# Optimization experiments

Hardware: AMD Instinct MI355X
Metric: run time of the kernel (lower is better)

## Reference

```python
import jax, jax.numpy as jnp
import numpy as np
from jax import lax

D, H_HEADS, DEPTH, E, HID, P, NCLS = 768, 12, 12, 4, 3072, 16, 1000

def _ln(x, w, b, eps=1e-5):
    m = x.mean(-1, keepdims=True)
    v = ((x - m) ** 2).mean(-1, keepdims=True)
    return (x - m) * lax.rsqrt(v + eps) * w + b

def setup_inputs() -> dict:
    key = jax.random.key(0)
    ks = jax.random.split(key, 16)
    s = 0.02
    inp = {
        'x': jax.random.normal(ks[0], (32, 3, 224, 224), jnp.float32),
        'conv_w': jax.random.normal(ks[1], (D, 3, P, P), jnp.float32) * s,
        'conv_b': jnp.zeros((D,), jnp.float32),
        'cls_token': jnp.zeros((1, 1, D), jnp.float32),
        'pos_embed': jax.random.normal(ks[2], (1, 197, D), jnp.float32) * s,
        'ln1_w': jnp.ones((DEPTH, D), jnp.float32),
        'ln1_b': jnp.zeros((DEPTH, D), jnp.float32),
        'qkv_w': jax.random.normal(ks[3], (DEPTH, 3 * D, D), jnp.float32) * s,
        'qkv_b': jnp.zeros((DEPTH, 3 * D), jnp.float32),
        'out_w': jax.random.normal(ks[4], (DEPTH, D, D), jnp.float32) * s,
        'out_b': jnp.zeros((DEPTH, D), jnp.float32),
        'ln2_w': jnp.ones((DEPTH, D), jnp.float32),
        'ln2_b': jnp.zeros((DEPTH, D), jnp.float32),
        'gate_w': jax.random.normal(ks[5], (DEPTH, E, D), jnp.float32) * s,
        'gate_b': jnp.zeros((DEPTH, E), jnp.float32),
        'e1_w': jax.random.normal(ks[6], (DEPTH, E, HID, D), jnp.float32) * s,
        'e1_b': jnp.zeros((DEPTH, E, HID), jnp.float32),
        'e2_w': jax.random.normal(ks[7], (DEPTH, E, D, HID), jnp.float32) * s,
        'e2_b': jnp.zeros((DEPTH, E, D), jnp.float32),
        'fnorm_w': jnp.ones((D,), jnp.float32),
        'fnorm_b': jnp.zeros((D,), jnp.float32),
        'head_w': jax.random.normal(ks[8], (NCLS, D), jnp.float32) * s,
        'head_b': jnp.zeros((NCLS,), jnp.float32),
    }
    return inp

def reference(x, conv_w, conv_b, cls_token, pos_embed, ln1_w, ln1_b, qkv_w, qkv_b,
              out_w, out_b, ln2_w, ln2_b, gate_w, gate_b, e1_w, e1_b, e2_w, e2_b,
              fnorm_w, fnorm_b, head_w, head_b):
    B = x.shape[0]
    # patch embedding: conv stride=patch, then flatten -> [B, N, D]
    x = lax.conv_general_dilated(x, conv_w, (P, P), 'VALID',
                                 dimension_numbers=('NCHW', 'OIHW', 'NCHW'))
    x = x + conv_b[None, :, None, None]
    x = x.reshape(B, D, -1).transpose(0, 2, 1)
    x = jnp.concatenate([jnp.broadcast_to(cls_token, (B, 1, D)), x], axis=1)
    x = x + pos_embed
    N = x.shape[1]
    hd = D // H_HEADS
    for i in range(DEPTH):
        # --- attention ---
        h = x
        y = _ln(x, ln1_w[i], ln1_b[i])
        qkv = y @ qkv_w[i].T + qkv_b[i]                      # [B,N,3D]
        q, k, v = jnp.split(qkv, 3, axis=-1)
        q = q.reshape(B, N, H_HEADS, hd).transpose(0, 2, 1, 3) / jnp.sqrt(hd).astype(x.dtype)
        k = k.reshape(B, N, H_HEADS, hd).transpose(0, 2, 1, 3)
        v = v.reshape(B, N, H_HEADS, hd).transpose(0, 2, 1, 3)
        attn = jax.nn.softmax(jnp.einsum('bhqd,bhkd->bhqk', q, k), axis=-1)
        ctx = jnp.einsum('bhqk,bhkd->bhqd', attn, v).transpose(0, 2, 1, 3).reshape(B, N, D)
        x = h + (ctx @ out_w[i].T + out_b[i])
        # --- MoE MLP (dense: all experts computed then masked, top_k=1) ---
        h = x
        y = _ln(x, ln2_w[i], ln2_b[i])
        gate = y @ gate_w[i].T + gate_b[i]                   # [B,N,E]
        topk_scores, topk_idx = lax.top_k(gate, 1)           # [B,N,1]
        score = jax.nn.softmax(topk_scores, axis=-1)[..., 0]  # [B,N] (==1 for k=1)
        h1 = jax.nn.gelu(jnp.einsum('bnd,ehd->benh', y, e1_w[i])
                         + e1_b[i][None, :, None, :], approximate=False)  # [B,E,N,HID]
        oe = jnp.einsum('benh,edh->bend', h1, e2_w[i]) + e2_b[i][None, :, None, :]
        mask = jax.nn.one_hot(topk_idx[..., 0], E, dtype=y.dtype)  # [B,N,E]
        moe = jnp.einsum('bne,bend->bnd', mask * score[..., None], oe)
        x = h + moe
    x = _ln(x, fnorm_w, fnorm_b)
    cls = x[:, 0]
    return cls @ head_w.T + head_b
```

## Files before the change

### kernel.cpp

```cpp
#include <hip/hip_runtime.h>
#include <hip/hip_bf16.h>
#include <math.h>

#define D_MODEL 768
#define SEQ     197
#define BATCH   32
#define NTOK    (BATCH*SEQ)
#define NHEAD   12
#define HDIM    64
#define NEXP    4
#define HID_N   3072
#define DEPTH_N 12

typedef __attribute__((ext_vector_type(4))) float f32x4;
typedef __attribute__((ext_vector_type(8))) short bf16x8;
typedef __attribute__((ext_vector_type(4))) unsigned short u16x4;
typedef unsigned short u16;

static __device__ __forceinline__ u16 f2bf(float f){
  unsigned int u = __builtin_bit_cast(unsigned int, f);
  u += 0x7FFFu + ((u >> 16) & 1u);
  return (u16)(u >> 16);
}
static __device__ __forceinline__ void split_bf(float x, u16& h, u16& l){
  h = f2bf(x);
  float hf = __builtin_bit_cast(float, (unsigned)h << 16);
  l = f2bf(x - hf);
}

static __device__ __forceinline__ float wred_sum(float v){
  #pragma unroll
  for (int off = 32; off; off >>= 1) v += __shfl_down(v, off);
  return v;
}

static __device__ __forceinline__ void gld16(const u16* g, u16* l){
  __builtin_amdgcn_global_load_lds(
      (const __attribute__((address_space(1))) unsigned int*)g,
      (__attribute__((address_space(3))) unsigned int*)l, 16, 0, 0);
}

__global__ __launch_bounds__(256) void split_many(const float* __restrict__ src,
                                                  u16* __restrict__ hi,
                                                  u16* __restrict__ lo, long n4){
  for (long i = blockIdx.x*256L + threadIdx.x; i < n4; i += (long)gridDim.x*256){
    f32x4 v = *reinterpret_cast<const f32x4*>(src + i*4);
    u16x4 h, l;
    #pragma unroll
    for (int j = 0; j < 4; j++){ u16 hh, ll; split_bf(v[j], hh, ll); h[j]=hh; l[j]=ll; }
    *reinterpret_cast<u16x4*>(hi + i*4) = h;
    *reinterpret_cast<u16x4*>(lo + i*4) = l;
  }
}

template<int MODE, int NG>
__global__ __launch_bounds__(256, 2) void gemm_split(
    const u16* __restrict__ Ahp, const u16* __restrict__ Alp,
    const u16* __restrict__ Whp, const u16* __restrict__ Wlp,
    const float* __restrict__ bias, const float* __restrict__ resid,
    float* __restrict__ C, const float* __restrict__ pos,
    u16* __restrict__ Chi, u16* __restrict__ Clo,
    const int* __restrict__ toks, const int* __restrict__ cnts,
    const int* __restrict__ offs, const int* __restrict__ tiles,
    int MTg, int NBg, int M, int N, int K)
{
  const int tid = threadIdx.x;
  const int NB = N >> 7;
  const int xcd = blockIdx.x & 7;
  const int idx = blockIdx.x >> 3;
  const int mg = xcd / NG, ng = xcd - mg*NG;
  const int mt = mg*MTg + idx / NBg;
  const int nb = ng*NBg + idx % NBg;
  if (nb >= NB) return;

  int cnt = M, base = 0, m0;
  if (MODE == 2 || MODE == 3){
    if (mt >= tiles[0]) return;
    const int e = tiles[1 + 2*mt];
    m0 = tiles[2 + 2*mt];
    cnt  = cnts[e];
    base = offs[e];
    Whp  += (size_t)e * N * K;
    Wlp  += (size_t)e * N * K;
    bias += (size_t)e * N;
  } else {
    m0 = mt * 128;
    if (m0 >= M) return;
  }
  const int n0 = nb * 128;

  __shared__ __align__(16) u16 lds[2][4][4096];

  const int lane = tid & 63, wid = tid >> 6;
  const int i0 = wid*128 + lane;
  const int r0 = i0 >> 2, r1 = r0 + 16;
  const int x0 = (i0 & 3) ^ ((r0 >> 1) & 3);
  const int x1 = (i0 & 3) ^ ((r1 >> 1) & 3);
  const int d0 = wid*1024, d1 = wid*1024 + 512;

  size_t aA0 = 0, aA1 = 0, pb0 = 0, pb1 = 0;
  {
    const int gm0 = m0 + r0, gm1 = m0 + r1;
    if (MODE == 0 || MODE == 1){
      aA0 = (size_t)(gm0 < M ? gm0 : 0) * K + x0*8;
      aA1 = (size_t)(gm1 < M ? gm1 : 0) * K + x1*8;
    }
    if (MODE == 2){
      aA0 = (size_t)(gm0 < cnt ? toks[base+gm0] : 0) * K + x0*8;
      aA1 = (size_t)(gm1 < cnt ? toks[base+gm1] : 0) * K + x1*8;
    }
    if (MODE == 3){
      aA0 = (size_t)(gm0 < cnt ? base+gm0 : 0) * K + x0*8;
      aA1 = (size_t)(gm1 < cnt ? base+gm1 : 0) * K + x1*8;
    }
    if (MODE == 4){
      int b_ = gm0 / 196, pp = gm0 - b_*196;
      pb0 = (size_t)b_*150528 + (size_t)(pp/14)*3584 + (size_t)(pp%14)*16;
      b_ = gm1 / 196; pp = gm1 - b_*196;
      pb1 = (size_t)b_*150528 + (size_t)(pp/14)*3584 + (size_t)(pp%14)*16;
    }
  }
  const size_t aW0 = (size_t)(n0 + r0) * K + x0*8;
  const size_t aW1 = (size_t)(n0 + r1) * K + x1*8;

  auto STAGE = [&](int buf, int t){
    const int k0 = t * 32;
    if (MODE == 4){
      const int kq0 = k0 + x0*8, kq1 = k0 + x1*8;
      size_t a0 = pb0 + (size_t)(kq0>>8)*50176 + (size_t)((kq0>>4)&15)*224 + (size_t)(kq0&15);
      size_t a1 = pb1 + (size_t)(kq1>>8)*50176 + (size_t)((kq1>>4)&15)*224 + (size_t)(kq1&15);
      gld16(Ahp + a0, &lds[buf][0][d0]); gld16(Ahp + a1, &lds[buf][0][d1]);
      gld16(Alp + a0, &lds[buf][1][d0]); gld16(Alp + a1, &lds[buf][1][d1]);
    } else {
      gld16(Ahp + aA0 + k0, &lds[buf][0][d0]); gld16(Ahp + aA1 + k0, &lds[buf][0][d1]);
      gld16(Alp + aA0 + k0, &lds[buf][1][d0]); gld16(Alp + aA1 + k0, &lds[buf][1][d1]);
    }
    gld16(Whp + aW0 + k0, &lds[buf][2][d0]); gld16(Whp + aW1 + k0, &lds[buf][2][d1]);
    gld16(Wlp + aW0 + k0, &lds[buf][3][d0]); gld16(Wlp + aW1 + k0, &lds[buf][3][d1]);
  };

  const int wr = wid >> 1, wc = wid & 1;
  const int lr = lane & 15, lq = lane >> 4;
  int cA[4], cW[4];
  #pragma unroll
  for (int mi = 0; mi < 4; mi++){
    int ra = wr*64 + mi*16 + lr;
    cA[mi] = (4*ra + (lq ^ ((ra>>1)&3))) * 8;
  }
  #pragma unroll
  for (int nj = 0; nj < 4; nj++){
    int rw = wc*64 + nj*16 + lr;
    cW[nj] = (4*rw + (lq ^ ((rw>>1)&3))) * 8;
  }

  const int NT = K >> 5;
  f32x4 acc[4][4] = {};

  STAGE(0, 0);
  for (int t = 0; t < NT; t++){
    const int buf = t & 1;
    if (t + 1 < NT){
      STAGE(buf ^ 1, t + 1);
      asm volatile("s_waitcnt vmcnt(8)" ::: "memory");
    } else {
      asm volatile("s_waitcnt vmcnt(0)" ::: "memory");
    }
    __builtin_amdgcn_s_barrier();
    asm volatile("" ::: "memory");
    const u16* L = &lds[buf][0][0];
    bf16x8 afh[4], afl[4], bfh[4], bfl[4];
    #pragma unroll
    for (int mi = 0; mi < 4; mi++){
      afh[mi] = *reinterpret_cast<const bf16x8*>(L + cA[mi]);
      afl[mi] = *reinterpret_cast<const bf16x8*>(L + 4096 + cA[mi]);
    }
    #pragma unroll
    for (int nj = 0; nj < 4; nj++){
      bfh[nj] = *reinterpret_cast<const bf16x8*>(L + 2*4096 + cW[nj]);
      bfl[nj] = *reinterpret_cast<const bf16x8*>(L + 3*4096 + cW[nj]);
    }
    #pragma unroll
    for (int mi = 0; mi < 4; mi++)
      #pragma unroll
      for (int nj = 0; nj < 4; nj++){
        acc[mi][nj] = __builtin_amdgcn_mfma_f32_16x16x32_bf16(afh[mi], bfh[nj], acc[mi][nj], 0, 0, 0);
        acc[mi][nj] = __builtin_amdgcn_mfma_f32_16x16x32_bf16(afh[mi], bfl[nj], acc[mi][nj], 0, 0, 0);
        acc[mi][nj] = __builtin_amdgcn_mfma_f32_16x16x32_bf16(afl[mi], bfh[nj], acc[mi][nj], 0, 0, 0);
      }
    asm volatile("" ::: "memory");
    __builtin_amdgcn_s_barrier();
  }

  #pragma unroll
  for (int nj = 0; nj < 4; nj++){
    const int ncol = n0 + wc*64 + nj*16 + lr;
    const float bv = bias[ncol];
    #pragma unroll
    for (int mi = 0; mi < 4; mi++){
      const int mb = m0 + wr*64 + mi*16 + lq*4;
      #pragma unroll
      for (int j = 0; j < 4; j++){
        const int m = mb + j;
        float v = acc[mi][nj][j] + bv;
        if (MODE == 0){
          if (m < M) C[(size_t)m * N + ncol] = v;
        }
        if (MODE == 1){
          if (m < M) C[(size_t)m * N + ncol] = v + resid[(size_t)m * N + ncol];
        }
        if (MODE == 2){
          if (m < cnt){
            v = 0.5f * v * (1.f + erff(v * 0.70710678118f));
            u16 h, l; split_bf(v, h, l);
            Chi[(size_t)(base + m) * N + ncol] = h;
            Clo[(size_t)(base + m) * N + ncol] = l;
          }
        }
        if (MODE == 3){
          if (m < cnt){
            int tok = toks[base + m];
            C[(size_t)tok * N + ncol] += v;
          }
        }
        if (MODE == 4){
          int b_ = m / 196, pp = m - b_ * 196;
          C[((size_t)b_ * 197 + 1 + pp) * D_MODEL + ncol] =
              v + pos[(size_t)(1 + pp) * D_MODEL + ncol];
        }
      }
    }
  }
}

__global__ __launch_bounds__(256) void cls_init(const float* __restrict__ cls_tk,
                                                const float* __restrict__ pos,
                                                float* __restrict__ xt){
  const int b = blockIdx.x, tid = threadIdx.x;
  for (int d = tid; d < D_MODEL; d += 256)
    xt[((size_t)b*SEQ)*D_MODEL + d] = cls_tk[d] + pos[d];
}

__global__ __launch_bounds__(256) void ln_kernel(const float* __restrict__ x, size_t xstride,
                                                 const float* __restrict__ w,
                                                 const float* __restrict__ b,
                                                 float* __restrict__ y, size_t ystride,
                                                 u16* __restrict__ yh, u16* __restrict__ yl){
  const int t = blockIdx.x;
  const int tid = threadIdx.x;
  const float* row = x + (size_t)t*xstride;
  float v0 = row[tid], v1 = row[tid+256], v2 = row[tid+512];
  __shared__ float red[4];
  float s = wred_sum(v0+v1+v2);
  if ((tid & 63) == 0) red[tid>>6] = s;
  __syncthreads();
  const float mean = (red[0]+red[1]+red[2]+red[3]) * (1.f/768.f);
  const float d0 = v0-mean, d1 = v1-mean, d2 = v2-mean;
  __syncthreads();
  float q = wred_sum(d0*d0 + d1*d1 + d2*d2);
  if ((tid & 63) == 0) red[tid>>6] = q;
  __syncthreads();
  const float var = (red[0]+red[1]+red[2]+red[3]) * (1.f/768.f);
  const float inv = rsqrtf(var + 1e-5f);
  float o0 = d0*inv*w[tid]     + b[tid];
  float o1 = d1*inv*w[tid+256] + b[tid+256];
  float o2 = d2*inv*w[tid+512] + b[tid+512];
  float* yr = y + (size_t)t*ystride;
  yr[tid] = o0; yr[tid+256] = o1; yr[tid+512] = o2;
  if (yh){
    u16 h, l;
    size_t rb = (size_t)t*768;
    split_bf(o0, h, l); yh[rb+tid]     = h; yl[rb+tid]     = l;
    split_bf(o1, h, l); yh[rb+tid+256] = h; yl[rb+tid+256] = l;
    split_bf(o2, h, l); yh[rb+tid+512] = h; yl[rb+tid+512] = l;
  }
}

__global__ __launch_bounds__(256, 3) void attn_f32(const float* __restrict__ qkv,
                                                   u16* __restrict__ ctxh,
                                                   u16* __restrict__ ctxl){
  const int qt = blockIdx.x, h = blockIdx.y, b = blockIdx.z;
  const int tid = threadIdx.x;
  const int tx = tid & 15, ty = tid >> 4;
  __shared__ float Qs[64][65];
  __shared__ float KPs[64][65];
  __shared__ float Vs[64][65];
  const size_t rs = 3*D_MODEL;
  const float* base = qkv + (size_t)b*SEQ*rs + (size_t)h*HDIM;

  #pragma unroll
  for (int it = 0; it < 16; it++){
    int idx = tid + it*256;
    int r = idx >> 6, c = idx & 63;
    int gq = qt*64 + r;
    float v = (gq < SEQ) ? base[(size_t)gq*rs + c] : 0.f;
    Qs[r][c] = v * 0.125f;
  }
  float m_run[4], l_run[4], o[4][4];
  #pragma unroll
  for (int i = 0; i < 4; i++){
    m_run[i] = -3.0e38f; l_run[i] = 0.f;
    #pragma unroll
    for (int j = 0; j < 4; j++) o[i][j] = 0.f;
  }
  __syncthreads();

  for (int kt = 0; kt < 4; kt++){
    #pragma unroll
    for (int it = 0; it < 16; it++){
      int idx = tid + it*256;
      int r = idx >> 6, c = idx & 63;
      int gk = kt*64 + r;
      float kv = (gk < SEQ) ? base[(size_t)gk*rs + D_MODEL   + c] : 0.f;
      float vv = (gk < SEQ) ? base[(size_t)gk*rs + 2*D_MODEL + c] : 0.f;
      KPs[r][c] = kv;
      Vs[r][c]  = vv;
    }
    __syncthreads();
    float s[4][4] = {};
    for (int d = 0; d < 64; d++){
      float qv[4], kv2[4];
      #pragma unroll
      for (int i = 0; i < 4; i++) qv[i]  = Qs[ty*4+i][d];
      #pragma unroll
      for (int j = 0; j < 4; j++) kv2[j] = KPs[tx*4+j][d];
      #pragma unroll
      for (int i = 0; i < 4; i++)
        #pragma unroll
        for (int j = 0; j < 4; j++) s[i][j] += qv[i]*kv2[j];
    }
    #pragma unroll
    for (int j = 0; j < 4; j++){
      if (kt*64 + tx*4 + j >= SEQ){
        #pragma unroll
        for (int i = 0; i < 4; i++) s[i][j] = -3.0e38f;
      }
    }
    float scale[4];
    #pragma unroll
    for (int i = 0; i < 4; i++){
      float mt = fmaxf(fmaxf(s[i][0], s[i][1]), fmaxf(s[i][2], s[i][3]));
      #pragma unroll
      for (int msk = 1; msk <= 8; msk <<= 1) mt = fmaxf(mt, __shfl_xor(mt, msk));
      float mnew = fmaxf(m_run[i], mt);
      scale[i] = __expf(m_run[i] - mnew);
      float ls = 0.f;
      #pragma unroll
      for (int j = 0; j < 4; j++){ s[i][j] = __expf(s[i][j] - mnew); ls += s[i][j]; }
      #pragma unroll
      for (int msk = 1; msk <= 8; msk <<= 1) ls += __shfl_xor(ls, msk);
      l_run[i] = l_run[i]*scale[i] + ls;
      m_run[i] = mnew;
    }
    __syncthreads();
    #pragma unroll
    for (int i = 0; i < 4; i++)
      #pragma unroll
      for (int j = 0; j < 4; j++) KPs[ty*4+i][tx*4+j] = s[i][j];
    __syncthreads();
    #pragma unroll
    for (int i = 0; i < 4; i++)
      #pragma unroll
      for (int j = 0; j < 4; j++) o[i][j] *= scale[i];
    for (int k = 0; k < 64; k++){
      float pv[4], vv[4];
      #pragma unroll
      for (int i = 0; i < 4; i++) pv[i] = KPs[ty*4+i][k];
      #pragma unroll
      for (int j = 0; j < 4; j++) vv[j] = Vs[k][tx*4+j];
      #pragma unroll
      for (int i = 0; i < 4; i++)
        #pragma unroll
        for (int j = 0; j < 4; j++) o[i][j] += pv[i]*vv[j];
    }
    __syncthreads();
  }
  #pragma unroll
  for (int i = 0; i < 4; i++){
    int q = qt*64 + ty*4 + i;
    if (q < SEQ){
      float inv = 1.f / l_run[i];
      #pragma unroll
      for (int j = 0; j < 4; j++){
        u16 hh, ll;
        split_bf(o[i][j]*inv, hh, ll);
        size_t idx = ((size_t)(b*SEQ + q))*D_MODEL + h*HDIM + tx*4 + j;
        ctxh[idx] = hh; ctxl[idx] = ll;
      }
    }
  }
}

__global__ __launch_bounds__(256) void gate_kernel(const float* __restrict__ y,
                                                   const float* __restrict__ gw,
                                                   const float* __restrict__ gb,
                                                   int* __restrict__ eidx,
                                                   int* __restrict__ counts){
  const int t = blockIdx.x;
  const int tid = threadIdx.x;
  const int e = tid >> 6, lane = tid & 63;
  const float* row = y + (size_t)t*D_MODEL;
  const float* wrow = gw + (size_t)e*D_MODEL;
  float acc = 0.f;
  for (int k = lane; k < D_MODEL; k += 64) acc += row[k]*wrow[k];
  acc = wred_sum(acc);
  __shared__ float sc[NEXP];
  if (lane == 0) sc[e] = acc + gb[e];
  __syncthreads();
  if (tid == 0){
    int best = 0; float bv = sc[0];
    #pragma unroll
    for (int k = 1; k < NEXP; k++) if (sc[k] > bv){ bv = sc[k]; best = k; }
    eidx[t] = best;
    atomicAdd(&counts[best], 1);
  }
}

__global__ void zero_counts(int* c){ if (threadIdx.x < 3*NEXP) c[threadIdx.x] = 0; }

__global__ void offsets_kernel(const int* counts, int* offs, int* cursor, int* tiles){
  if (threadIdx.x == 0){
    int o = 0, n = 0;
    for (int e = 0; e < NEXP; e++){
      offs[e] = o; cursor[e] = o;
      for (int m0 = 0; m0 < counts[e]; m0 += 128){
        tiles[1+2*n] = e; tiles[2+2*n] = m0; n++;
      }
      o += counts[e];
    }
    tiles[0] = n;
  }
}

__global__ __launch_bounds__(256) void scatter_kernel(const int* __restrict__ eidx,
                                                      int* cursor, int* __restrict__ toks){
  int i = blockIdx.x*256 + threadIdx.x;
  if (i < NTOK){ int pos = atomicAdd(&cursor[eidx[i]], 1); toks[pos] = i; }
}

__global__ __launch_bounds__(256) void gemm_f32(const float* __restrict__ A,
                                                const float* __restrict__ W,
                                                const float* __restrict__ bias,
                                                const float* __restrict__ resid,
                                                float* __restrict__ C,
                                                int M, int N, int K){
  const int m0 = blockIdx.x*64, bn = blockIdx.y*64;
  const int tid = threadIdx.x;
  const int tx = tid & 15, ty = tid >> 4;
  __shared__ float As[16][65];
  __shared__ float Ws[16][65];
  float acc[4][4] = {};
  for (int k0 = 0; k0 < K; k0 += 16){
    #pragma unroll
    for (int i = 0; i < 4; i++){
      int idx = tid + i*256;
      int k = idx & 15, m = idx >> 4;
      As[k][m] = (m0+m < M) ? A[(size_t)(m0+m)*K + k0 + k] : 0.f;
      Ws[k][m] = (bn+m < N) ? W[(size_t)(bn+m)*K + k0 + k] : 0.f;
    }
    __syncthreads();
    #pragma unroll
    for (int kk = 0; kk < 16; kk++){
      float a0 = As[kk][ty*4+0], a1 = As[kk][ty*4+1], a2 = As[kk][ty*4+2], a3 = As[kk][ty*4+3];
      float w0 = Ws[kk][tx*4+0], w1 = Ws[kk][tx*4+1], w2 = Ws[kk][tx*4+2], w3 = Ws[kk][tx*4+3];
      acc[0][0] += a0*w0; acc[0][1] += a0*w1; acc[0][2] += a0*w2; acc[0][3] += a0*w3;
      acc[1][0] += a1*w0; acc[1][1] += a1*w1; acc[1][2] += a1*w2; acc[1][3] += a1*w3;
      acc[2][0] += a2*w0; acc[2][1] += a2*w1; acc[2][2] += a2*w2; acc[2][3] += a2*w3;
      acc[3][0] += a3*w0; acc[3][1] += a3*w1; acc[3][2] += a3*w2; acc[3][3] += a3*w3;
    }
    __syncthreads();
  }
  #pragma unroll
  for (int i = 0; i < 4; i++){
    int m = m0 + ty*4 + i;
    if (m >= M) continue;
    #pragma unroll
    for (int j = 0; j < 4; j++){
      int n = bn + tx*4 + j;
      if (n >= N) continue;
      float v = acc[i][j];
      if (bias)  v += bias[n];
      if (resid) v += resid[(size_t)m*N + n];
      C[(size_t)m*N + n] = v;
    }
  }
}

extern "C" void kernel_launch(void* const* d_in, const int* in_sizes, int n_in,
                              void* d_out, int out_size, void* d_ws, size_t ws_size,
                              hipStream_t stream){
  const float* x      = (const float*)d_in[0];
  const float* conv_w = (const float*)d_in[1];
  const float* conv_b = (const float*)d_in[2];
  const float* cls_tk = (const float*)d_in[3];
  const float* pos    = (const float*)d_in[4];
  const float* ln1w   = (const float*)d_in[5];
  const float* ln1b   = (const float*)d_in[6];
  const float* qkvw   = (const float*)d_in[7];
  const float* qkvb   = (const float*)d_in[8];
  const float* outw   = (const float*)d_in[9];
  const float* outb   = (const float*)d_in[10];
  const float* ln2w   = (const float*)d_in[11];
  const float* ln2b   = (const float*)d_in[12];
  const float* gatew  = (const float*)d_in[13];
  const float* gateb  = (const float*)d_in[14];
  const float* e1w    = (const float*)d_in[15];
  const float* e1b    = (const float*)d_in[16];
  const float* e2w    = (const float*)d_in[17];
  const float* e2b    = (const float*)d_in[18];
  const float* fnw    = (const float*)d_in[19];
  const float* fnb    = (const float*)d_in[20];
  const float* headw  = (const float*)d_in[21];
  const float* headb  = (const float*)d_in[22];
  float* out = (float*)d_out;

  float* ws    = (float*)d_ws;
  float* xt    = ws;
  float* y     = xt  + (size_t)NTOK*D_MODEL;
  float* qkv   = y   + (size_t)NTOK*D_MODEL;
  float* clsln = qkv + (size_t)NTOK*3*D_MODEL;
  int*   eidx   = (int*)(clsln + (size_t)BATCH*D_MODEL);
  int*   toks   = eidx + NTOK;
  int*   counts = toks + NTOK;
  int*   offs   = counts + NEXP;
  int*   cursor = offs + NEXP;
  int*   tiles  = cursor + NEXP;
  u16* up = (u16*)(((size_t)(tiles + 120) + 15) & ~(size_t)15);
  const size_t nY  = (size_t)NTOK*D_MODEL;
  const size_t nH1 = (size_t)NTOK*HID_N;
  const size_t nX  = (size_t)BATCH*3*224*224;
  const size_t nCW = 768*768;
  const size_t nQW = (size_t)DEPTH_N*3*D_MODEL*D_MODEL;
  const size_t nOW = (size_t)DEPTH_N*D_MODEL*D_MODEL;
  const size_t nE1 = (size_t)DEPTH_N*NEXP*HID_N*D_MODEL;
  const size_t nE2 = (size_t)DEPTH_N*NEXP*D_MODEL*HID_N;
  u16 *yh = up,      *yl = yh + nY;
  u16 *ch = yl + nY, *cl = ch + nY;
  u16 *h1h = cl + nY, *h1l = h1h + nH1;
  u16 *xh = h1l + nH1, *xl = xh + nX;
  u16 *cwh = xl + nX,  *cwl = cwh + nCW;
  u16 *qwh = cwl + nCW, *qwl = qwh + nQW;
  u16 *owh = qwl + nQW, *owl = owh + nOW;
  u16 *e1h = owl + nOW, *e1l = e1h + nE1;
  u16 *e2h = e1l + nE1, *e2l = e2h + nE2;

  dim3 b256(256);

  split_many<<<2048, b256, 0, stream>>>(x,      xh,  xl,  (long)(nX/4));
  split_many<<<2048, b256, 0, stream>>>(conv_w, cwh, cwl, (long)(nCW/4));
  split_many<<<2048, b256, 0, stream>>>(qkvw,   qwh, qwl, (long)(nQW/4));
  split_many<<<2048, b256, 0, stream>>>(outw,   owh, owl, (long)(nOW/4));
  split_many<<<2048, b256, 0, stream>>>(e1w,    e1h, e1l, (long)(nE1/4));
  split_many<<<2048, b256, 0, stream>>>(e2w,    e2h, e2l, (long)(nE2/4));

  gemm_split<4,2><<<dim3(8*13*3), b256, 0, stream>>>(xh, xl, cwh, cwl,
      conv_b, nullptr, xt, pos, nullptr, nullptr,
      nullptr, nullptr, nullptr, nullptr, 13, 3, 6272, D_MODEL, 768);
  cls_init<<<dim3(BATCH), b256, 0, stream>>>(cls_tk, pos, xt);

  for (int i = 0; i < DEPTH_N; i++){
    ln_kernel<<<dim3(NTOK), b256, 0, stream>>>(xt, D_MODEL,
        ln1w + (size_t)i*D_MODEL, ln1b + (size_t)i*D_MODEL, y, D_MODEL, yh, yl);
    gemm_split<0,2><<<dim3(8*13*9), b256, 0, stream>>>(yh, yl,
        qwh + (size_t)i*3*D_MODEL*D_MODEL, qwl + (size_t)i*3*D_MODEL*D_MODEL,
        qkvb + (size_t)i*3*D_MODEL, nullptr, qkv, nullptr, nullptr, nullptr,
        nullptr, nullptr, nullptr, nullptr, 13, 9, NTOK, 3*D_MODEL, D_MODEL);
    attn_f32<<<dim3(4, NHEAD, BATCH), b256, 0, stream>>>(qkv, ch, cl);
    gemm_split<1,2><<<dim3(8*13*3), b256, 0, stream>>>(ch, cl,
        owh + (size_t)i*D_MODEL*D_MODEL, owl + (size_t)i*D_MODEL*D_MODEL,
        outb + (size_t)i*D_MODEL, xt, xt, nullptr, nullptr, nullptr,
        nullptr, nullptr, nullptr, nullptr, 13, 3, NTOK, D_MODEL, D_MODEL);
    ln_kernel<<<dim3(NTOK), b256, 0, stream>>>(xt, D_MODEL,
        ln2w + (size_t)i*D_MODEL, ln2b + (size_t)i*D_MODEL, y, D_MODEL, yh, yl);
    zero_counts<<<1, 64, 0, stream>>>(counts);
    gate_kernel<<<dim3(NTOK), b256, 0, stream>>>(y,
        gatew + (size_t)i*NEXP*D_MODEL, gateb + (size_t)i*NEXP, eidx, counts);
    offsets_kernel<<<1, 64, 0, stream>>>(counts, offs, cursor, tiles);
    scatter_kernel<<<dim3((NTOK+255)/256), b256, 0, stream>>>(eidx, cursor, toks);
    gemm_split<2,4><<<dim3(8*27*6), b256, 0, stream>>>(yh, yl,
        e1h + (size_t)i*NEXP*HID_N*D_MODEL, e1l + (size_t)i*NEXP*HID_N*D_MODEL,
        e1b + (size_t)i*NEXP*HID_N, nullptr, nullptr, nullptr, h1h, h1l,
        toks, counts, offs, tiles, 27, 6, NTOK, HID_N, D_MODEL);
    gemm_split<3,2><<<dim3(8*14*3), b256, 0, stream>>>(h1h, h1l,
        e2h + (size_t)i*NEXP*D_MODEL*HID_N, e2l + (size_t)i*NEXP*D_MODEL*HID_N,
        e2b + (size_t)i*NEXP*D_MODEL, nullptr, xt, nullptr, nullptr, nullptr,
        toks, counts, offs, tiles, 14, 3, NTOK, D_MODEL, HID_N);
  }

  ln_kernel<<<dim3(BATCH), b256, 0, stream>>>(xt, (size_t)SEQ*D_MODEL, fnw, fnb,
      clsln, D_MODEL, nullptr, nullptr);
  gemm_f32<<<dim3(1, 16), b256, 0, stream>>>(clsln, headw, headb, nullptr, out, BATCH, 1000, D_MODEL);
}
```

Baseline: 10.62 ms.

## Fuse MoE expert up-projection, GELU and down-projection into one kernel

Replaces the two grouped expert GEMM launches with a single moe_ffn kernel. Each block owns a 32-token tile of one expert, keeps the gathered activations in LDS, and loops over 128-wide hidden chunks: it computes the up-projection, applies GELU, keeps the split-bf16 result in LDS, and accumulates the down-projection in registers before scatter-adding into the residual. The goal is to drop the large hidden-activation buffer and its round trip through global memory. In exchange, expert weights are read straight from global memory by every 32-row tile with no LDS staging, which raises weight traffic several-fold. The kernel also runs one 256-thread block per CU with a fixed 224-block grid, which limits latency hiding.

```diff
diff --git a/kernel.cpp b/kernel.cpp
--- a/kernel.cpp
+++ b/kernel.cpp
@@ -59,9 +59,6 @@
     const u16* __restrict__ Whp, const u16* __restrict__ Wlp,
     const float* __restrict__ bias, const float* __restrict__ resid,
     float* __restrict__ C, const float* __restrict__ pos,
-    u16* __restrict__ Chi, u16* __restrict__ Clo,
-    const int* __restrict__ toks, const int* __restrict__ cnts,
-    const int* __restrict__ offs, const int* __restrict__ tiles,
     int MTg, int NBg, int M, int N, int K)
 {
   const int tid = threadIdx.x;
@@ -72,21 +69,8 @@
   const int mt = mg*MTg + idx / NBg;
   const int nb = ng*NBg + idx % NBg;
   if (nb >= NB) return;
-
-  int cnt = M, base = 0, m0;
-  if (MODE == 2 || MODE == 3){
-    if (mt >= tiles[0]) return;
-    const int e = tiles[1 + 2*mt];
-    m0 = tiles[2 + 2*mt];
-    cnt  = cnts[e];
-    base = offs[e];
-    Whp  += (size_t)e * N * K;
-    Wlp  += (size_t)e * N * K;
-    bias += (size_t)e * N;
-  } else {
-    m0 = mt * 128;
-    if (m0 >= M) return;
-  }
+  const int m0 = mt * 128;
+  if (m0 >= M) return;
   const int n0 = nb * 128;
 
   __shared__ __align__(16) u16 lds[2][4][4096];
@@ -104,14 +88,6 @@
     if (MODE == 0 || MODE == 1){
       aA0 = (size_t)(gm0 < M ? gm0 : 0) * K + x0*8;
       aA1 = (size_t)(gm1 < M ? gm1 : 0) * K + x1*8;
-    }
-    if (MODE == 2){
-      aA0 = (size_t)(gm0 < cnt ? toks[base+gm0] : 0) * K + x0*8;
-      aA1 = (size_t)(gm1 < cnt ? toks[base+gm1] : 0) * K + x1*8;
-    }
-    if (MODE == 3){
-      aA0 = (size_t)(gm0 < cnt ? base+gm0 : 0) * K + x0*8;
-      aA1 = (size_t)(gm1 < cnt ? base+gm1 : 0) * K + x1*8;
     }
     if (MODE == 4){
       int b_ = gm0 / 196, pp = gm0 - b_*196;
@@ -208,20 +184,6 @@
         if (MODE == 1){
           if (m < M) C[(size_t)m * N + ncol] = v + resid[(size_t)m * N + ncol];
         }
-        if (MODE == 2){
-          if (m < cnt){
-            v = 0.5f * v * (1.f + erff(v * 0.70710678118f));
-            u16 h, l; split_bf(v, h, l);
-            Chi[(size_t)(base + m) * N + ncol] = h;
-            Clo[(size_t)(base + m) * N + ncol] = l;
-          }
-        }
-        if (MODE == 3){
-          if (m < cnt){
-            int tok = toks[base + m];
-            C[(size_t)tok * N + ncol] += v;
-          }
-        }
         if (MODE == 4){
           int b_ = m / 196, pp = m - b_ * 196;
           C[((size_t)b_ * 197 + 1 + pp) * D_MODEL + ncol] =
@@ -229,6 +191,133 @@
         }
       }
     }
+  }
+}
+
+__global__ __launch_bounds__(256, 1) void moe_ffn(
+    const u16* __restrict__ Yh, const u16* __restrict__ Yl,
+    const u16* __restrict__ W1h, const u16* __restrict__ W1l,
+    const u16* __restrict__ W2h, const u16* __restrict__ W2l,
+    const float* __restrict__ b1, const float* __restrict__ b2,
+    float* __restrict__ xt,
+    const int* __restrict__ toks, const int* __restrict__ cnts,
+    const int* __restrict__ offs, const int* __restrict__ tiles)
+{
+  const int tid = threadIdx.x;
+  const int lane = tid & 63, wid = tid >> 6;
+  const int tile = (blockIdx.x & 7)*28 + (blockIdx.x >> 3);
+  if (tile >= tiles[0]) return;
+  const int e  = tiles[1 + 2*tile];
+  const int m0 = tiles[2 + 2*tile];
+  const int cnt = cnts[e], base = offs[e];
+  W1h += (size_t)e*HID_N*D_MODEL; W1l += (size_t)e*HID_N*D_MODEL;
+  W2h += (size_t)e*D_MODEL*HID_N; W2l += (size_t)e*D_MODEL*HID_N;
+  b1  += (size_t)e*HID_N;         b2  += (size_t)e*D_MODEL;
+
+  __shared__ __align__(16) u16 Ys[2][32*768];
+  __shared__ __align__(16) u16 Gs[2][2][32*128];
+
+  #pragma unroll
+  for (int p = 0; p < 2; p++){
+    const u16* src = p ? Yl : Yh;
+    #pragma unroll
+    for (int g = 0; g < 12; g++){
+      int c = (wid*12 + g)*64 + lane;
+      int row = c / 96, jp = c - row*96;
+      int j = jp ^ (row & 7);
+      int gm = m0 + row;
+      int tok = toks[base + (gm < cnt ? gm : 0)];
+      gld16(src + (size_t)tok*768 + j*8, &Ys[p][(size_t)(wid*12 + g)*512]);
+    }
+  }
+  asm volatile("s_waitcnt vmcnt(0)" ::: "memory");
+  __syncthreads();
+
+  const int lr = lane & 15, lq = lane >> 4;
+  f32x4 acc[2][12] = {};
+
+  for (int hc = 0; hc < 24; hc++){
+    const int gb = hc & 1;
+    f32x4 s[2][2] = {};
+    for (int t = 0; t < 24; t++){
+      bf16x8 ah[2], al[2], bh[2], bl[2];
+      #pragma unroll
+      for (int mf = 0; mf < 2; mf++){
+        int row = lr + 16*mf;
+        int off = (row*96 + ((t*4 + lq) ^ (lr & 7)))*8;
+        ah[mf] = *reinterpret_cast<const bf16x8*>(&Ys[0][off]);
+        al[mf] = *reinterpret_cast<const bf16x8*>(&Ys[1][off]);
+      }
+      #pragma unroll
+      for (int nf = 0; nf < 2; nf++){
+        size_t wo = (size_t)(hc*128 + wid*32 + nf*16 + lr)*768 + t*32 + lq*8;
+        bh[nf] = *reinterpret_cast<const bf16x8*>(W1h + wo);
+        bl[nf] = *reinterpret_cast<const bf16x8*>(W1l + wo);
+      }
+      #pragma unroll
+      for (int mf = 0; mf < 2; mf++)
+        #pragma unroll
+        for (int nf = 0; nf < 2; nf++){
+          s[mf][nf] = __builtin_amdgcn_mfma_f32_16x16x32_bf16(ah[mf], bh[nf], s[mf][nf], 0, 0, 0);
+          s[mf][nf] = __builtin_amdgcn_mfma_f32_16x16x32_bf16(ah[mf], bl[nf], s[mf][nf], 0, 0, 0);
+          s[mf][nf] = __builtin_amdgcn_mfma_f32_16x16x32_bf16(al[mf], bh[nf], s[mf][nf], 0, 0, 0);
+        }
+    }
+    #pragma unroll
+    for (int mf = 0; mf < 2; mf++)
+      #pragma unroll
+      for (int nf = 0; nf < 2; nf++){
+        int coll = wid*32 + nf*16 + lr;
+        float bv = b1[hc*128 + coll];
+        #pragma unroll
+        for (int r = 0; r < 4; r++){
+          int row = mf*16 + lq*4 + r;
+          float v = s[mf][nf][r] + bv;
+          v = 0.5f*v*(1.f + erff(v*0.70710678118f));
+          u16 h, l; split_bf(v, h, l);
+          int ci = (row*16 + ((coll >> 3) ^ (row & 7)))*8 + (coll & 7);
+          Gs[gb][0][ci] = h; Gs[gb][1][ci] = l;
+        }
+      }
+    __syncthreads();
+    for (int ks = 0; ks < 4; ks++){
+      bf16x8 gah[2], gal[2];
+      #pragma unroll
+      for (int mf = 0; mf < 2; mf++){
+        int row = lr + 16*mf;
+        int off = (row*16 + ((ks*4 + lq) ^ (lr & 7)))*8;
+        gah[mf] = *reinterpret_cast<const bf16x8*>(&Gs[gb][0][off]);
+        gal[mf] = *reinterpret_cast<const bf16x8*>(&Gs[gb][1][off]);
+      }
+      #pragma unroll
+      for (int nf = 0; nf < 12; nf++){
+        size_t wo = (size_t)(wid*192 + nf*16 + lr)*3072 + hc*128 + ks*32 + lq*8;
+        bf16x8 bh = *reinterpret_cast<const bf16x8*>(W2h + wo);
+        bf16x8 bl = *reinterpret_cast<const bf16x8*>(W2l + wo);
+        #pragma unroll
+        for (int mf = 0; mf < 2; mf++){
+          acc[mf][nf] = __builtin_amdgcn_mfma_f32_16x16x32_bf16(gah[mf], bh, acc[mf][nf], 0, 0, 0);
+          acc[mf][nf] = __builtin_amdgcn_mfma_f32_16x16x32_bf16(gah[mf], bl, acc[mf][nf], 0, 0, 0);
+          acc[mf][nf] = __builtin_amdgcn_mfma_f32_16x16x32_bf16(gal[mf], bh, acc[mf][nf], 0, 0, 0);
+        }
+      }
+    }
+  }
+
+  #pragma unroll
+  for (int nf = 0; nf < 12; nf++){
+    int col = wid*192 + nf*16 + lr;
+    float bv = b2[col];
+    #pragma unroll
+    for (int mf = 0; mf < 2; mf++)
+      #pragma unroll
+      for (int r = 0; r < 4; r++){
+        int m = mf*16 + lq*4 + r;
+        if (m0 + m < cnt){
+          int tok = toks[base + m0 + m];
+          xt[(size_t)tok*768 + col] += acc[mf][nf][r] + bv;
+        }
+      }
   }
 }
 
@@ -422,7 +511,7 @@
     int o = 0, n = 0;
     for (int e = 0; e < NEXP; e++){
       offs[e] = o; cursor[e] = o;
-      for (int m0 = 0; m0 < counts[e]; m0 += 128){
+      for (int m0 = 0; m0 < counts[e]; m0 += 32){
         tiles[1+2*n] = e; tiles[2+2*n] = m0; n++;
       }
       o += counts[e];
@@ -524,9 +613,8 @@
   int*   offs   = counts + NEXP;
   int*   cursor = offs + NEXP;
   int*   tiles  = cursor + NEXP;
-  u16* up = (u16*)(((size_t)(tiles + 120) + 15) & ~(size_t)15);
+  u16* up = (u16*)(((size_t)(tiles + 512) + 15) & ~(size_t)15);
   const size_t nY  = (size_t)NTOK*D_MODEL;
-  const size_t nH1 = (size_t)NTOK*HID_N;
   const size_t nX  = (size_t)BATCH*3*224*224;
   const size_t nCW = 768*768;
   const size_t nQW = (size_t)DEPTH_N*3*D_MODEL*D_MODEL;
@@ -535,8 +623,7 @@
   const size_t nE2 = (size_t)DEPTH_N*NEXP*D_MODEL*HID_N;
   u16 *yh = up,      *yl = yh + nY;
   u16 *ch = yl + nY, *cl = ch + nY;
-  u16 *h1h = cl + nY, *h1l = h1h + nH1;
-  u16 *xh = h1l + nH1, *xl = xh + nX;
+  u16 *xh = cl + nY,  *xl = xh + nX;
   u16 *cwh = xl + nX,  *cwl = cwh + nCW;
   u16 *qwh = cwl + nCW, *qwl = qwh + nQW;
   u16 *owh = qwl + nQW, *owl = owh + nOW;
@@ -553,8 +640,7 @@
   split_many<<<2048, b256, 0, stream>>>(e2w,    e2h, e2l, (long)(nE2/4));
 
   gemm_split<4,2><<<dim3(8*13*3), b256, 0, stream>>>(xh, xl, cwh, cwl,
-      conv_b, nullptr, xt, pos, nullptr, nullptr,
-      nullptr, nullptr, nullptr, nullptr, 13, 3, 6272, D_MODEL, 768);
+      conv_b, nullptr, xt, pos, 13, 3, 6272, D_MODEL, 768);
   cls_init<<<dim3(BATCH), b256, 0, stream>>>(cls_tk, pos, xt);
 
   for (int i = 0; i < DEPTH_N; i++){
@@ -562,13 +648,13 @@
         ln1w + (size_t)i*D_MODEL, ln1b + (size_t)i*D_MODEL, y, D_MODEL, yh, yl);
     gemm_split<0,2><<<dim3(8*13*9), b256, 0, stream>>>(yh, yl,
         qwh + (size_t)i*3*D_MODEL*D_MODEL, qwl + (size_t)i*3*D_MODEL*D_MODEL,
-        qkvb + (size_t)i*3*D_MODEL, nullptr, qkv, nullptr, nullptr, nullptr,
-        nullptr, nullptr, nullptr, nullptr, 13, 9, NTOK, 3*D_MODEL, D_MODEL);
+        qkvb + (size_t)i*3*D_MODEL, nullptr, qkv, nullptr,
+        13, 9, NTOK, 3*D_MODEL, D_MODEL);
     attn_f32<<<dim3(4, NHEAD, BATCH), b256, 0, stream>>>(qkv, ch, cl);
     gemm_split<1,2><<<dim3(8*13*3), b256, 0, stream>>>(ch, cl,
         owh + (size_t)i*D_MODEL*D_MODEL, owl + (size_t)i*D_MODEL*D_MODEL,
-        outb + (size_t)i*D_MODEL, xt, xt, nullptr, nullptr, nullptr,
-        nullptr, nullptr, nullptr, nullptr, 13, 3, NTOK, D_MODEL, D_MODEL);
+        outb + (size_t)i*D_MODEL, xt, xt, nullptr,
+        13, 3, NTOK, D_MODEL, D_MODEL);
     ln_kernel<<<dim3(NTOK), b256, 0, stream>>>(xt, D_MODEL,
         ln2w + (size_t)i*D_MODEL, ln2b + (size_t)i*D_MODEL, y, D_MODEL, yh, yl);
     zero_counts<<<1, 64, 0, stream>>>(counts);
@@ -576,14 +662,11 @@
         gatew + (size_t)i*NEXP*D_MODEL, gateb + (size_t)i*NEXP, eidx, counts);
     offsets_kernel<<<1, 64, 0, stream>>>(counts, offs, cursor, tiles);
     scatter_kernel<<<dim3((NTOK+255)/256), b256, 0, stream>>>(eidx, cursor, toks);
-    gemm_split<2,4><<<dim3(8*27*6), b256, 0, stream>>>(yh, yl,
+    moe_ffn<<<dim3(224), b256, 0, stream>>>(yh, yl,
         e1h + (size_t)i*NEXP*HID_N*D_MODEL, e1l + (size_t)i*NEXP*HID_N*D_MODEL,
-        e1b + (size_t)i*NEXP*HID_N, nullptr, nullptr, nullptr, h1h, h1l,
-        toks, counts, offs, tiles, 27, 6, NTOK, HID_N, D_MODEL);
-    gemm_split<3,2><<<dim3(8*14*3), b256, 0, stream>>>(h1h, h1l,
         e2h + (size_t)i*NEXP*D_MODEL*HID_N, e2l + (size_t)i*NEXP*D_MODEL*HID_N,
-        e2b + (size_t)i*NEXP*D_MODEL, nullptr, xt, nullptr, nullptr, nullptr,
-        toks, counts, offs, tiles, 14, 3, NTOK, D_MODEL, HID_N);
+        e1b + (size_t)i*NEXP*HID_N, e2b + (size_t)i*NEXP*D_MODEL,
+        xt, toks, counts, offs, tiles);
   }
 
   ln_kernel<<<dim3(BATCH), b256, 0, stream>>>(xt, (size_t)SEQ*D_MODEL, fnw, fnb,
```

Result: slower. 18.55 ms (+74.7%).

## Triple-buffer weight tiles in split-bf16 GEMM and fold count zeroing into LN

Applied to the files above, without the earlier changes.

The GEMM now prefetches weight tiles two K-steps ahead using a three-slot LDS ring, while activations stay double-buffered. The aim is to hide more global-load latency on the weight stream. In exchange LDS use per block goes from 64KB to 80KB, which may lower occupancy. The LN kernel also skips the fp32 output when it is not needed (LN1) and zeroes the expert counters itself, which removes the zero_counts launch.

```diff
diff --git a/kernel.cpp b/kernel.cpp
--- a/kernel.cpp
+++ b/kernel.cpp
@@ -89,7 +89,8 @@
   }
   const int n0 = nb * 128;
 
-  __shared__ __align__(16) u16 lds[2][4][4096];
+  __shared__ __align__(16) u16 Alds[2][2][4096];
+  __shared__ __align__(16) u16 Wlds[3][2][4096];
 
   const int lane = tid & 63, wid = tid >> 6;
   const int i0 = wid*128 + lane;
@@ -123,20 +124,23 @@
   const size_t aW0 = (size_t)(n0 + r0) * K + x0*8;
   const size_t aW1 = (size_t)(n0 + r1) * K + x1*8;
 
-  auto STAGE = [&](int buf, int t){
+  auto STAGE_A = [&](int buf, int t){
     const int k0 = t * 32;
     if (MODE == 4){
       const int kq0 = k0 + x0*8, kq1 = k0 + x1*8;
       size_t a0 = pb0 + (size_t)(kq0>>8)*50176 + (size_t)((kq0>>4)&15)*224 + (size_t)(kq0&15);
       size_t a1 = pb1 + (size_t)(kq1>>8)*50176 + (size_t)((kq1>>4)&15)*224 + (size_t)(kq1&15);
-      gld16(Ahp + a0, &lds[buf][0][d0]); gld16(Ahp + a1, &lds[buf][0][d1]);
-      gld16(Alp + a0, &lds[buf][1][d0]); gld16(Alp + a1, &lds[buf][1][d1]);
+      gld16(Ahp + a0, &Alds[buf][0][d0]); gld16(Ahp + a1, &Alds[buf][0][d1]);
+      gld16(Alp + a0, &Alds[buf][1][d0]); gld16(Alp + a1, &Alds[buf][1][d1]);
     } else {
-      gld16(Ahp + aA0 + k0, &lds[buf][0][d0]); gld16(Ahp + aA1 + k0, &lds[buf][0][d1]);
-      gld16(Alp + aA0 + k0, &lds[buf][1][d0]); gld16(Alp + aA1 + k0, &lds[buf][1][d1]);
-    }
-    gld16(Whp + aW0 + k0, &lds[buf][2][d0]); gld16(Whp + aW1 + k0, &lds[buf][2][d1]);
-    gld16(Wlp + aW0 + k0, &lds[buf][3][d0]); gld16(Wlp + aW1 + k0, &lds[buf][3][d1]);
+      gld16(Ahp + aA0 + k0, &Alds[buf][0][d0]); gld16(Ahp + aA1 + k0, &Alds[buf][0][d1]);
+      gld16(Alp + aA0 + k0, &Alds[buf][1][d0]); gld16(Alp + aA1 + k0, &Alds[buf][1][d1]);
+    }
+  };
+  auto STAGE_W = [&](int buf, int t){
+    const int k0 = t * 32;
+    gld16(Whp + aW0 + k0, &Wlds[buf][0][d0]); gld16(Whp + aW1 + k0, &Wlds[buf][0][d1]);
+    gld16(Wlp + aW0 + k0, &Wlds[buf][1][d0]); gld16(Wlp + aW1 + k0, &Wlds[buf][1][d1]);
   };
 
   const int wr = wid >> 1, wc = wid & 1;
@@ -156,28 +160,35 @@
   const int NT = K >> 5;
   f32x4 acc[4][4] = {};
 
-  STAGE(0, 0);
+  STAGE_A(0, 0);
+  STAGE_W(0, 0);
+  if (NT > 1) STAGE_W(1, 1);
+
+  int wb = 0;
   for (int t = 0; t < NT; t++){
-    const int buf = t & 1;
-    if (t + 1 < NT){
-      STAGE(buf ^ 1, t + 1);
+    const int abuf = t & 1;
+    if (t + 2 < NT){
+      STAGE_A(abuf ^ 1, t + 1);
+      STAGE_W(wb == 0 ? 2 : wb - 1, t + 2);
+      asm volatile("s_waitcnt vmcnt(12)" ::: "memory");
+    } else if (t + 1 < NT){
+      STAGE_A(abuf ^ 1, t + 1);
       asm volatile("s_waitcnt vmcnt(8)" ::: "memory");
     } else {
       asm volatile("s_waitcnt vmcnt(0)" ::: "memory");
     }
     __builtin_amdgcn_s_barrier();
     asm volatile("" ::: "memory");
-    const u16* L = &lds[buf][0][0];
     bf16x8 afh[4], afl[4], bfh[4], bfl[4];
     #pragma unroll
     for (int mi = 0; mi < 4; mi++){
-      afh[mi] = *reinterpret_cast<const bf16x8*>(L + cA[mi]);
-      afl[mi] = *reinterpret_cast<const bf16x8*>(L + 4096 + cA[mi]);
+      afh[mi] = *reinterpret_cast<const bf16x8*>(&Alds[abuf][0][cA[mi]]);
+      afl[mi] = *reinterpret_cast<const bf16x8*>(&Alds[abuf][1][cA[mi]]);
     }
     #pragma unroll
     for (int nj = 0; nj < 4; nj++){
-      bfh[nj] = *reinterpret_cast<const bf16x8*>(L + 2*4096 + cW[nj]);
-      bfl[nj] = *reinterpret_cast<const bf16x8*>(L + 3*4096 + cW[nj]);
+      bfh[nj] = *reinterpret_cast<const bf16x8*>(&Wlds[wb][0][cW[nj]]);
+      bfl[nj] = *reinterpret_cast<const bf16x8*>(&Wlds[wb][1][cW[nj]]);
     }
     #pragma unroll
     for (int mi = 0; mi < 4; mi++)
@@ -189,6 +200,7 @@
       }
     asm volatile("" ::: "memory");
     __builtin_amdgcn_s_barrier();
+    wb = (wb == 2) ? 0 : wb + 1;
   }
 
   #pragma unroll
@@ -244,9 +256,11 @@
                                                  const float* __restrict__ w,
                                                  const float* __restrict__ b,
                                                  float* __restrict__ y, size_t ystride,
-                                                 u16* __restrict__ yh, u16* __restrict__ yl){
+                                                 u16* __restrict__ yh, u16* __restrict__ yl,
+                                                 int* __restrict__ zero4){
   const int t = blockIdx.x;
   const int tid = threadIdx.x;
+  if (zero4 && t == 0 && tid < NEXP) zero4[tid] = 0;
   const float* row = x + (size_t)t*xstride;
   float v0 = row[tid], v1 = row[tid+256], v2 = row[tid+512];
   __shared__ float red[4];
@@ -264,8 +278,10 @@
   float o0 = d0*inv*w[tid]     + b[tid];
   float o1 = d1*inv*w[tid+256] + b[tid+256];
   float o2 = d2*inv*w[tid+512] + b[tid+512];
-  float* yr = y + (size_t)t*ystride;
-  yr[tid] = o0; yr[tid+256] = o1; yr[tid+512] = o2;
+  if (y){
+    float* yr = y + (size_t)t*ystride;
+    yr[tid] = o0; yr[tid+256] = o1; yr[tid+512] = o2;
+  }
   if (yh){
     u16 h, l;
     size_t rb = (size_t)t*768;
@@ -414,8 +430,6 @@
     atomicAdd(&counts[best], 1);
   }
 }
-
-__global__ void zero_counts(int* c){ if (threadIdx.x < 3*NEXP) c[threadIdx.x] = 0; }
 
 __global__ void offsets_kernel(const int* counts, int* offs, int* cursor, int* tiles){
   if (threadIdx.x == 0){
@@ -559,7 +573,8 @@
 
   for (int i = 0; i < DEPTH_N; i++){
     ln_kernel<<<dim3(NTOK), b256, 0, stream>>>(xt, D_MODEL,
-        ln1w + (size_t)i*D_MODEL, ln1b + (size_t)i*D_MODEL, y, D_MODEL, yh, yl);
+        ln1w + (size_t)i*D_MODEL, ln1b + (size_t)i*D_MODEL,
+        nullptr, D_MODEL, yh, yl, nullptr);
     gemm_split<0,2><<<dim3(8*13*9), b256, 0, stream>>>(yh, yl,
         qwh + (size_t)i*3*D_MODEL*D_MODEL, qwl + (size_t)i*3*D_MODEL*D_MODEL,
         qkvb + (size_t)i*3*D_MODEL, nullptr, qkv, nullptr, nullptr, nullptr,
@@ -570,8 +585,8 @@
         outb + (size_t)i*D_MODEL, xt, xt, nullptr, nullptr, nullptr,
         nullptr, nullptr, nullptr, nullptr, 13, 3, NTOK, D_MODEL, D_MODEL);
     ln_kernel<<<dim3(NTOK), b256, 0, stream>>>(xt, D_MODEL,
-        ln2w + (size_t)i*D_MODEL, ln2b + (size_t)i*D_MODEL, y, D_MODEL, yh, yl);
-    zero_counts<<<1, 64, 0, stream>>>(counts);
+        ln2w + (size_t)i*D_MODEL, ln2b + (size_t)i*D_MODEL,
+        y, D_MODEL, yh, yl, counts);
     gate_kernel<<<dim3(NTOK), b256, 0, stream>>>(y,
         gatew + (size_t)i*NEXP*D_MODEL, gateb + (size_t)i*NEXP, eidx, counts);
     offsets_kernel<<<1, 64, 0, stream>>>(counts, offs, cursor, tiles);
@@ -587,6 +602,6 @@
   }
 
   ln_kernel<<<dim3(BATCH), b256, 0, stream>>>(xt, (size_t)SEQ*D_MODEL, fnw, fnb,
-      clsln, D_MODEL, nullptr, nullptr);
+      clsln, D_MODEL, nullptr, nullptr, nullptr);
   gemm_f32<<<dim3(1, 16), b256, 0, stream>>>(clsln, headw, headb, nullptr, out, BATCH, 1000, D_MODEL);
 }
```

Result: no change. 10.79 ms (+1.6%).
